# Kernel tuning notes

Hardware: AMD Instinct MI355X
Metric: run time of the kernel (lower is better)

Reference implementation:

```python
import jax, jax.numpy as jnp
import numpy as np


def _conv(x, w, pad):
    return jax.lax.conv_general_dilated(x, w, (1, 1), [(pad, pad), (pad, pad)],
                                        dimension_numbers=('NCHW', 'OIHW', 'NCHW'))


def _cbs(x, w, s, b, pad):
    # Conv + (folded inference BatchNorm as per-channel affine) + SiLU
    y = _conv(x, w, pad) * s[None, :, None, None] + b[None, :, None, None]
    return y * jax.nn.sigmoid(y)


def _pixel_shuffle(x, r):
    N, C, H, W = x.shape
    c = C // (r * r)
    return x.reshape(N, c, r, r, H, W).transpose(0, 1, 4, 2, 5, 3).reshape(N, c, H * r, W * r)


def _pixel_unshuffle(x, r):
    N, C, H, W = x.shape
    h, w = H // r, W // r
    return x.reshape(N, C, h, r, w, r).transpose(0, 1, 3, 5, 2, 4).reshape(N, C * r * r, h, w)


def _carafe(x, dw, db, ew, eb, k, up):
    # Content-aware reassembly: predict per-pixel k*k kernels for up*up sub-positions,
    # softmax-normalize, then gather-multiply-accumulate over k*k neighborhoods.
    N, C, H, W = x.shape
    kt = _conv(x, dw, 0) + db[None, :, None, None]
    if k % 2 == 0:
        kt = jnp.pad(kt, ((0, 0), (0, 0), (k // 2, k // 2 - 1), (k // 2, k // 2 - 1)))
        kt = _conv(kt, ew, 0) + eb[None, :, None, None]
    else:
        kt = _conv(kt, ew, k // 2) + eb[None, :, None, None]
    kt = _pixel_shuffle(kt, up)                     # [N, k*k, H*up, W*up]
    kt = jax.nn.softmax(kt, axis=1)
    # non-overlapping unfold(step=up) -> [N, H, W, k*k, up*up]
    kt = kt.reshape(N, k * k, H, up, W, up).transpose(0, 2, 4, 1, 3, 5).reshape(N, H, W, k * k, up * up)
    if k % 2 == 0:
        xp = jnp.pad(x, ((0, 0), (0, 0), (k // 2, k // 2 - 1), (k // 2, k // 2 - 1)))
    else:
        xp = jnp.pad(x, ((0, 0), (0, 0), (k // 2, k // 2), (k // 2, k // 2)))
    # k*k sliding patches (k is a small static constant)
    patches = jnp.stack([xp[:, :, i:i + H, j:j + W] for i in range(k) for j in range(k)], axis=-1)
    patches = patches.transpose(0, 2, 3, 1, 4)      # [N, H, W, C, k*k]
    out = jnp.einsum('nhwck,nhwkr->nhwcr', patches, kt)  # [N, H, W, C, up*up]
    out = out.reshape(N, H, W, C * up * up).transpose(0, 3, 1, 2)
    return _pixel_shuffle(out, up)


def _forward(x, cv1_w, cv1_s, cv1_b, m1a_w, m1a_s, m1a_b, m1b_w, m1b_s, m1b_b,
             cvm2_w, cvm2_s, cvm2_b, u2_down_w, u2_down_b, u2_enc_w, u2_enc_b,
             m2a_w, m2a_s, m2a_b, m2b_w, m2b_s, m2b_b,
             cvm3_w, cvm3_s, cvm3_b, u3_down_w, u3_down_b, u3_enc_w, u3_enc_b,
             m3a_w, m3a_s, m3a_b, m3b_w, m3b_s, m3b_b, cv2_w, cv2_s, cv2_b):
    C = cv1_w.shape[0] // 2
    t = _cbs(x, cv1_w, cv1_s, cv1_b, 0)
    y, y0 = t[:, :C], t[:, C:]

    def bneck(z, wa, sa, ba, wb, sb, bb):  # shortcut=False, e=1.0
        return _cbs(_cbs(z, wa, sa, ba, 1), wb, sb, bb, 1)

    y1 = bneck(y0, m1a_w, m1a_s, m1a_b, m1b_w, m1b_s, m1b_b)
    y2 = _cbs(_pixel_unshuffle(y1, 2), cvm2_w, cvm2_s, cvm2_b, 0)
    y2 = _carafe(y2, u2_down_w, u2_down_b, u2_enc_w, u2_enc_b, 1, 2) + y1
    y2 = bneck(y2, m2a_w, m2a_s, m2a_b, m2b_w, m2b_s, m2b_b)
    y3 = _cbs(_pixel_unshuffle(y2, 4), cvm3_w, cvm3_s, cvm3_b, 0)
    y3 = _carafe(y3, u3_down_w, u3_down_b, u3_enc_w, u3_enc_b, 2, 4) + y2
    y3 = bneck(y3, m3a_w, m3a_s, m3a_b, m3b_w, m3b_s, m3b_b)
    return _cbs(jnp.concatenate([y, y0, y1, y2, y3], axis=1), cv2_w, cv2_s, cv2_b, 0)


def setup_inputs() -> dict:
    key = jax.random.key(0)
    ks = jax.random.split(key, 16)
    C = 128

    def cbs_p(k, co, ci, ksz):
        k1, k2, k3 = jax.random.split(k, 3)
        w = jax.random.normal(k1, (co, ci, ksz, ksz), jnp.float32) / np.sqrt(ci * ksz * ksz).astype(np.float32)
        s = 1.0 + 0.1 * jax.random.normal(k2, (co,), jnp.float32)
        b = 0.1 * jax.random.normal(k3, (co,), jnp.float32)
        return w, s, b

    d = {}
    d['x'] = jax.random.normal(ks[0], (8, 256, 128, 128), jnp.float32)
    d['cv1_w'], d['cv1_s'], d['cv1_b'] = cbs_p(ks[1], 2 * C, 256, 1)
    for name, kk in (('m1', ks[2]), ('m2', ks[3]), ('m3', ks[4])):
        ka, kb = jax.random.split(kk)
        d[name + 'a_w'], d[name + 'a_s'], d[name + 'a_b'] = cbs_p(ka, C, C, 3)
        d[name + 'b_w'], d[name + 'b_s'], d[name + 'b_b'] = cbs_p(kb, C, C, 3)
    d['cvm2_w'], d['cvm2_s'], d['cvm2_b'] = cbs_p(ks[5], C, 4 * C, 1)
    d['cvm3_w'], d['cvm3_s'], d['cvm3_b'] = cbs_p(ks[6], C, 16 * C, 1)
    d['u2_down_w'] = jax.random.normal(ks[7], (C // 4, C, 1, 1), jnp.float32) / np.sqrt(C).astype(np.float32)
    d['u2_down_b'] = 0.1 * jax.random.normal(ks[8], (C // 4,), jnp.float32)
    d['u2_enc_w'] = jax.random.normal(ks[9], (4, C // 4, 1, 1), jnp.float32) / np.sqrt(C // 4).astype(np.float32)
    d['u2_enc_b'] = 0.1 * jax.random.normal(ks[10], (4,), jnp.float32)
    d['u3_down_w'] = jax.random.normal(ks[11], (C // 4, C, 1, 1), jnp.float32) / np.sqrt(C).astype(np.float32)
    d['u3_down_b'] = 0.1 * jax.random.normal(ks[12], (C // 4,), jnp.float32)
    d['u3_enc_w'] = jax.random.normal(ks[13], (64, C // 4, 2, 2), jnp.float32) / np.sqrt((C // 4) * 4).astype(np.float32)
    d['u3_enc_b'] = 0.1 * jax.random.normal(ks[14], (64,), jnp.float32)
    d['cv2_w'], d['cv2_s'], d['cv2_b'] = cbs_p(ks[15], 256, 5 * C, 1)
    return d


def reference(x, cv1_w, cv1_s, cv1_b, m1a_w, m1a_s, m1a_b, m1b_w, m1b_s, m1b_b,
              cvm2_w, cvm2_s, cvm2_b, u2_down_w, u2_down_b, u2_enc_w, u2_enc_b,
              m2a_w, m2a_s, m2a_b, m2b_w, m2b_s, m2b_b,
              cvm3_w, cvm3_s, cvm3_b, u3_down_w, u3_down_b, u3_enc_w, u3_enc_b,
              m3a_w, m3a_s, m3a_b, m3b_w, m3b_s, m3b_b, cv2_w, cv2_s, cv2_b):
    return _forward(x, cv1_w, cv1_s, cv1_b, m1a_w, m1a_s, m1a_b, m1b_w, m1b_s, m1b_b,
                    cvm2_w, cvm2_s, cvm2_b, u2_down_w, u2_down_b, u2_enc_w, u2_enc_b,
                    m2a_w, m2a_s, m2a_b, m2b_w, m2b_s, m2b_b,
                    cvm3_w, cvm3_s, cvm3_b, u3_down_w, u3_down_b, u3_enc_w, u3_enc_b,
                    m3a_w, m3a_s, m3a_b, m3b_w, m3b_s, m3b_b, cv2_w, cv2_s, cv2_b)
```

## Files before the change

kernel.cpp:

```cpp
#include <hip/hip_runtime.h>

typedef unsigned short u16;
typedef short v8s __attribute__((ext_vector_type(8)));
typedef u16 v8u __attribute__((ext_vector_type(8)));
typedef float v4f __attribute__((ext_vector_type(4)));
typedef __bf16 v8bf __attribute__((ext_vector_type(8)));

__device__ __forceinline__ float bf2f(u16 u) {
    unsigned x = ((unsigned)u) << 16; float f; __builtin_memcpy(&f, &x, 4); return f;
}
__device__ __forceinline__ u16 f2bf(float f) {
    unsigned x; __builtin_memcpy(&x, &f, 4);
    x = x + 0x7FFFu + ((x >> 16) & 1u);
    return (u16)(x >> 16);
}
__device__ __forceinline__ float silu(float v) { return v / (1.f + __expf(-v)); }

__device__ __forceinline__ void gld16(const void* g, void* l) {
    __builtin_amdgcn_global_load_lds(
        (const __attribute__((address_space(1))) unsigned int*)(uintptr_t)g,
        (__attribute__((address_space(3))) unsigned int*)(unsigned int)(uintptr_t)l,
        16, 0, 0);
}

__global__ void cvtw(const float* __restrict__ in, u16* __restrict__ out, int n) {
    int i = blockIdx.x * 256 + threadIdx.x;
    if (i < n) out[i] = f2bf(in[i]);
}
__global__ void wtrans3(const float* __restrict__ in, u16* __restrict__ out) {
    int i = blockIdx.x * 256 + threadIdx.x;
    if (i >= 147456) return;
    int tap = i % 9; int rem = i / 9; int ci = rem & 127; int co = rem >> 7;
    out[((tap * 128 + co) << 7) + ci] = f2bf(in[i]);
}
__global__ void wtrans_ps(const float* __restrict__ in, u16* __restrict__ out, int R2) {
    int i = blockIdx.x * 256 + threadIdx.x;
    int tap = i % R2; int rem = i / R2; int c = rem & 127; int co = rem >> 7;
    out[((tap * 128 + co) << 7) + c] = f2bf(in[i]);
}

__global__ __launch_bounds__(256) void nchw2nhwc(const float* __restrict__ in, u16* __restrict__ out) {
    __shared__ u16 tile[64][72];
    const int n = blockIdx.z, c0 = blockIdx.y * 64, p0 = blockIdx.x * 64;
#pragma unroll
    for (int rep = 0; rep < 16; ++rep) {
        int idx = rep * 256 + threadIdx.x;
        int c = idx >> 6, p = idx & 63;
        tile[c][p] = f2bf(in[((size_t)(n * 256 + c0 + c)) * 16384 + p0 + p]);
    }
    __syncthreads();
#pragma unroll
    for (int rep = 0; rep < 16; ++rep) {
        int idx = rep * 256 + threadIdx.x;
        int p = idx >> 6, c = idx & 63;
        out[((size_t)n * 16384 + p0 + p) * 256 + c0 + c] = tile[c][p];
    }
}

__global__ __launch_bounds__(256, 3) void conv3_mfma(
    const u16* __restrict__ src, int c0, int srcC,
    const u16* __restrict__ wt,
    const float* __restrict__ scale, const float* __restrict__ bias,
    u16* __restrict__ out) {
    __shared__ u16 lds[2][3][128][32];
    const int n = blockIdx.y, h = blockIdx.x;
    const int tid = threadIdx.x;
    const int lane = tid & 63;
    const int wv = tid >> 6;
    const int r = lane & 15, q = lane >> 4;
    const int wr = wv >> 1, wc = wv & 1;

    v4f acc[4][4];
#pragma unroll
    for (int a = 0; a < 4; ++a)
#pragma unroll
        for (int b = 0; b < 4; ++b) acc[a][b] = (v4f){0.f, 0.f, 0.f, 0.f};

    const size_t rowstride = (size_t)128 * srcC;
    const u16* nbase = src + (size_t)n * 128 * rowstride + c0;

    auto stage = [&](int buf, int k0) {
#pragma unroll
        for (int kh = 0; kh < 3; ++kh) {
            int hh = h + kh - 1;
            char* dst0 = (char*)&lds[buf][kh][0][0];
            if ((unsigned)hh < 128u) {
                const u16* g = nbase + (size_t)hh * rowstride + k0;
#pragma unroll
                for (int j = 0; j < 2; ++j) {
                    int o = j * 4096 + tid * 16;
                    int s2 = o ^ ((o >> 3) & 0x70);
                    int px = s2 >> 6, cb = s2 & 63;
                    gld16((const char*)(g + (size_t)px * srcC) + cb,
                          dst0 + j * 4096 + wv * 1024);
                }
            } else {
#pragma unroll
                for (int j = 0; j < 2; ++j)
                    *(v8s*)(dst0 + j * 4096 + tid * 16) = (v8s){0, 0, 0, 0, 0, 0, 0, 0};
            }
        }
    };

    stage(0, 0);
    int buf = 0;
    for (int k0 = 0; k0 < 128; k0 += 32, buf ^= 1) {
        __syncthreads();
        if (k0 + 32 < 128) stage(buf ^ 1, k0 + 32);

        const u16* wk = wt + (size_t)(wc * 64 + r) * 128 + k0 + q * 8;
        v8bf bcur[4];
#pragma unroll
        for (int nt = 0; nt < 4; ++nt)
            bcur[nt] = __builtin_bit_cast(v8bf, *(const v8s*)(wk + nt * 2048));

#pragma unroll
        for (int tap = 0; tap < 9; ++tap) {
            const int kh = tap / 3, kw = tap % 3;
            v8bf afr[4];
#pragma unroll
            for (int mt = 0; mt < 4; ++mt) {
                int p = wr * 64 + mt * 16 + r + kw - 1;
                bool vp = (unsigned)p < 128u;
                int pc = vp ? p : 0;
                int ba = pc * 64 + q * 16;
                ba ^= (ba >> 3) & 0x70;
                v8s av = *(const v8s*)((const char*)&lds[buf][kh][0][0] + ba);
                if (!vp) av = (v8s){0, 0, 0, 0, 0, 0, 0, 0};
                afr[mt] = __builtin_bit_cast(v8bf, av);
            }
            v8bf bnxt[4];
            if (tap < 8) {
#pragma unroll
                for (int nt = 0; nt < 4; ++nt)
                    bnxt[nt] = __builtin_bit_cast(v8bf,
                        *(const v8s*)(wk + (size_t)(tap + 1) * 16384 + nt * 2048));
            }
#pragma unroll
            for (int mt = 0; mt < 4; ++mt)
#pragma unroll
                for (int nt = 0; nt < 4; ++nt)
                    acc[mt][nt] = __builtin_amdgcn_mfma_f32_16x16x32_bf16(
                        afr[mt], bcur[nt], acc[mt][nt], 0, 0, 0);
            if (tap < 8) {
#pragma unroll
                for (int nt = 0; nt < 4; ++nt) bcur[nt] = bnxt[nt];
            }
        }
    }

    const size_t obase = ((size_t)n * 128 + h) * 128;
#pragma unroll
    for (int nt = 0; nt < 4; ++nt) {
        int co = wc * 64 + nt * 16 + r;
        float s = scale[co], bi = bias[co];
#pragma unroll
        for (int mt = 0; mt < 4; ++mt) {
            int p = wr * 64 + mt * 16 + q * 4;
#pragma unroll
            for (int i = 0; i < 4; ++i) {
                float v = acc[mt][nt][i] * s + bi;
                out[(obase + p + i) * 128 + co] = f2bf(silu(v));
            }
        }
    }
}

__global__ __launch_bounds__(256) void conv1_mfma(
    const u16* __restrict__ src, int srcC,
    const u16* __restrict__ wt,
    const float* __restrict__ scale, const float* __restrict__ bias,
    u16* __restrict__ out, int Cout) {
    __shared__ u16 lds[2][128][64];
    const int n = blockIdx.z, co0 = blockIdx.y * 128, px0 = blockIdx.x * 128;
    const int tid = threadIdx.x;
    const int lane = tid & 63, wv = tid >> 6;
    const int r = lane & 15, q = lane >> 4;
    const int wr = wv >> 1, wc = wv & 1;

    v4f acc[4][4];
#pragma unroll
    for (int a = 0; a < 4; ++a)
#pragma unroll
        for (int b = 0; b < 4; ++b) acc[a][b] = (v4f){0.f, 0.f, 0.f, 0.f};

    const u16* abase = src + ((size_t)n * 16384 + px0) * srcC;

    auto stage = [&](int buf, int k0) {
#pragma unroll
        for (int j = 0; j < 4; ++j) {
            int o = j * 4096 + tid * 16;
            int s2 = o ^ ((o >> 3) & 0x70);
            int px = s2 >> 7, cb = s2 & 127;
            gld16((const char*)(abase + (size_t)px * srcC + k0) + cb,
                  (char*)&lds[buf][0][0] + j * 4096 + wv * 1024);
        }
    };

    stage(0, 0);
    int buf = 0;
    for (int k0 = 0; k0 < srcC; k0 += 64, buf ^= 1) {
        __syncthreads();
        if (k0 + 64 < srcC) stage(buf ^ 1, k0 + 64);

        const u16* wrow = wt + (size_t)(co0 + wc * 64 + r) * srcC + k0 + q * 8;
        v8bf bfr[2][4];
#pragma unroll
        for (int s = 0; s < 2; ++s)
#pragma unroll
            for (int nt = 0; nt < 4; ++nt)
                bfr[s][nt] = __builtin_bit_cast(v8bf,
                    *(const v8s*)(wrow + s * 32 + (size_t)nt * 16 * srcC));
#pragma unroll
        for (int s = 0; s < 2; ++s) {
            v8bf afr[4];
#pragma unroll
            for (int mt = 0; mt < 4; ++mt) {
                int ba = (wr * 64 + mt * 16 + r) * 128 + s * 64 + q * 16;
                ba ^= (ba >> 3) & 0x70;
                afr[mt] = __builtin_bit_cast(v8bf,
                    *(const v8s*)((const char*)&lds[buf][0][0] + ba));
            }
#pragma unroll
            for (int mt = 0; mt < 4; ++mt)
#pragma unroll
                for (int nt = 0; nt < 4; ++nt)
                    acc[mt][nt] = __builtin_amdgcn_mfma_f32_16x16x32_bf16(
                        afr[mt], bfr[s][nt], acc[mt][nt], 0, 0, 0);
        }
    }

#pragma unroll
    for (int nt = 0; nt < 4; ++nt) {
        int co = co0 + wc * 64 + nt * 16 + r;
        float s = scale[co], bi = bias[co];
#pragma unroll
        for (int mt = 0; mt < 4; ++mt) {
            int p = px0 + wr * 64 + mt * 16 + q * 4;
#pragma unroll
            for (int i = 0; i < 4; ++i) {
                float v = acc[mt][nt][i] * s + bi;
                out[((size_t)n * 16384 + p + i) * Cout + co] = f2bf(silu(v));
            }
        }
    }
}

__global__ __launch_bounds__(256) void cat_mfma(
    const u16* __restrict__ s0, const u16* __restrict__ s1,
    const u16* __restrict__ s2, const u16* __restrict__ s3,
    const u16* __restrict__ wt,
    const float* __restrict__ scale, const float* __restrict__ bias,
    float* __restrict__ out) {
    __shared__ u16 lds[2][128][64];
    const int n = blockIdx.z, co0 = blockIdx.y * 128, px0 = blockIdx.x * 128;
    const int tid = threadIdx.x;
    const int lane = tid & 63, wv = tid >> 6;
    const int r = lane & 15, q = lane >> 4;
    const int wr = wv >> 1, wc = wv & 1;

    v4f acc[4][4];
#pragma unroll
    for (int a = 0; a < 4; ++a)
#pragma unroll
        for (int b = 0; b < 4; ++b) acc[a][b] = (v4f){0.f, 0.f, 0.f, 0.f};

    const u16* srcs[4] = {s0, s1, s2, s3};
    const int sCq[4] = {256, 128, 128, 128};
    const int kbq[4] = {0, 256, 384, 512};
    const int segs[10] = {0, 0, 0, 0, 1, 1, 2, 2, 3, 3};
    const int k0s[10] = {0, 64, 128, 192, 0, 64, 0, 64, 0, 64};

    auto stage = [&](int buf, int c) {
        int seg = segs[c]; int sc = sCq[seg]; int k0 = k0s[c];
        const u16* ab = srcs[seg] + ((size_t)n * 16384 + px0) * sc;
#pragma unroll
        for (int j = 0; j < 4; ++j) {
            int o = j * 4096 + tid * 16;
            int s2 = o ^ ((o >> 3) & 0x70);
            int px = s2 >> 7, cb = s2 & 127;
            gld16((const char*)(ab + (size_t)px * sc + k0) + cb,
                  (char*)&lds[buf][0][0] + j * 4096 + wv * 1024);
        }
    };

    stage(0, 0);
    int buf = 0;
#pragma unroll
    for (int c = 0; c < 10; ++c, buf ^= 1) {
        __syncthreads();
        if (c < 9) stage(buf ^ 1, c + 1);

        const int seg = segs[c], k0 = k0s[c];
        const u16* wrow = wt + (size_t)(co0 + wc * 64 + r) * 640 + kbq[seg] + k0 + q * 8;
        v8bf bfr[2][4];
#pragma unroll
        for (int s = 0; s < 2; ++s)
#pragma unroll
            for (int nt = 0; nt < 4; ++nt)
                bfr[s][nt] = __builtin_bit_cast(v8bf,
                    *(const v8s*)(wrow + s * 32 + (size_t)nt * 16 * 640));
#pragma unroll
        for (int s = 0; s < 2; ++s) {
            v8bf afr[4];
#pragma unroll
            for (int mt = 0; mt < 4; ++mt) {
                int ba = (wr * 64 + mt * 16 + r) * 128 + s * 64 + q * 16;
                ba ^= (ba >> 3) & 0x70;
                afr[mt] = __builtin_bit_cast(v8bf,
                    *(const v8s*)((const char*)&lds[buf][0][0] + ba));
            }
#pragma unroll
            for (int mt = 0; mt < 4; ++mt)
#pragma unroll
                for (int nt = 0; nt < 4; ++nt)
                    acc[mt][nt] = __builtin_amdgcn_mfma_f32_16x16x32_bf16(
                        afr[mt], bfr[s][nt], acc[mt][nt], 0, 0, 0);
        }
    }

#pragma unroll
    for (int nt = 0; nt < 4; ++nt) {
        int co = co0 + wc * 64 + nt * 16 + r;
        float s = scale[co], bi = bias[co];
#pragma unroll
        for (int mt = 0; mt < 4; ++mt) {
            int p = px0 + wr * 64 + mt * 16 + q * 4;
            v4f o;
#pragma unroll
            for (int i = 0; i < 4; ++i) o[i] = silu(acc[mt][nt][i] * s + bi);
            *(v4f*)(out + (size_t)(n * 256 + co) * 16384 + p) = o;
        }
    }
}

template <int KH, int KW, int S, int PAD, int CIN>
__global__ __launch_bounds__(256) void conv_mfma(
    const u16* __restrict__ src, int c0, int srcC,
    const u16* __restrict__ wt,
    const float* __restrict__ scale, const float* __restrict__ bias,
    u16* __restrict__ out, int Hin, int Win, int Wout, int Cout) {
    const int n = blockIdx.z;
    const int co0 = blockIdx.y * 64;
    const int hw0 = blockIdx.x * 64;
    const int tid = threadIdx.x;
    const int lane = tid & 63, wv = tid >> 6;
    const int r = lane & 15, q = lane >> 4;
    const int wr = wv >> 1, wc = wv & 1;

    const int m0 = hw0 + wr * 32 + r;
    const int m1 = m0 + 16;
    const int h0 = m0 / Wout, w0 = m0 - h0 * Wout;
    const int h1 = m1 / Wout, w1 = m1 - h1 * Wout;

    v4f acc00 = {0.f, 0.f, 0.f, 0.f}, acc01 = {0.f, 0.f, 0.f, 0.f};
    v4f acc10 = {0.f, 0.f, 0.f, 0.f}, acc11 = {0.f, 0.f, 0.f, 0.f};

    const u16* b0base = wt + (size_t)(co0 + wc * 32 + r) * CIN + q * 8;
    const size_t wtap = (size_t)Cout * CIN;

    int tap = 0;
#pragma unroll
    for (int kh = 0; kh < KH; ++kh)
#pragma unroll
        for (int kw = 0; kw < KW; ++kw, ++tap) {
            int ih0 = h0 * S + kh - PAD, iw0 = w0 * S + kw - PAD;
            int ih1 = h1 * S + kh - PAD, iw1 = w1 * S + kw - PAD;
            bool v0 = ((unsigned)ih0 < (unsigned)Hin) & ((unsigned)iw0 < (unsigned)Win);
            bool v1 = ((unsigned)ih1 < (unsigned)Hin) & ((unsigned)iw1 < (unsigned)Win);
            int p0i = v0 ? (n * Hin + ih0) * Win + iw0 : 0;
            int p1i = v1 ? (n * Hin + ih1) * Win + iw1 : 0;
            const u16* a0 = src + (size_t)p0i * srcC + c0 + q * 8;
            const u16* a1 = src + (size_t)p1i * srcC + c0 + q * 8;
            const u16* b0 = b0base + (size_t)tap * wtap;
            const u16* b1 = b0 + (size_t)16 * CIN;
#pragma unroll
            for (int k = 0; k < CIN; k += 32) {
                v8s za = {0, 0, 0, 0, 0, 0, 0, 0};
                v8s a0s = za, a1s = za;
                if (v0) a0s = *(const v8s*)(a0 + k);
                if (v1) a1s = *(const v8s*)(a1 + k);
                v8s b0s = *(const v8s*)(b0 + k);
                v8s b1s = *(const v8s*)(b1 + k);
                v8bf af0 = __builtin_bit_cast(v8bf, a0s);
                v8bf af1 = __builtin_bit_cast(v8bf, a1s);
                v8bf bw0 = __builtin_bit_cast(v8bf, b0s);
                v8bf bw1 = __builtin_bit_cast(v8bf, b1s);
                acc00 = __builtin_amdgcn_mfma_f32_16x16x32_bf16(af0, bw0, acc00, 0, 0, 0);
                acc01 = __builtin_amdgcn_mfma_f32_16x16x32_bf16(af0, bw1, acc01, 0, 0, 0);
                acc10 = __builtin_amdgcn_mfma_f32_16x16x32_bf16(af1, bw0, acc10, 0, 0, 0);
                acc11 = __builtin_amdgcn_mfma_f32_16x16x32_bf16(af1, bw1, acc11, 0, 0, 0);
            }
        }

    const int HWo = gridDim.x * 64;
#pragma unroll
    for (int ct = 0; ct < 2; ++ct) {
        v4f av0 = ct ? acc01 : acc00;
        v4f av1 = ct ? acc11 : acc10;
        int co = co0 + wc * 32 + ct * 16 + r;
        float s = scale[co], bb = bias[co];
        int mb = hw0 + wr * 32 + q * 4;
#pragma unroll
        for (int i = 0; i < 4; ++i) {
            float x0 = av0[i] * s + bb;
            float x1 = av1[i] * s + bb;
            out[((size_t)n * HWo + mb + i) * Cout + co] = f2bf(silu(x0));
            out[((size_t)n * HWo + mb + 16 + i) * Cout + co] = f2bf(silu(x1));
        }
    }
}

__global__ __launch_bounds__(256) void k_upadd(const u16* __restrict__ y2a,
                                               const u16* __restrict__ y1,
                                               u16* __restrict__ out) {
    int t = blockIdx.x * 256 + threadIdx.x;
    int cg = t & 15; int pix = t >> 4;
    int n = pix >> 14; int p = pix & 16383; int ho = p >> 7; int wo = p & 127;
    const u16* a = y2a + ((size_t)((n * 64 + (ho >> 1)) * 64 + (wo >> 1))) * 128 + cg * 8;
    const u16* b = y1 + (size_t)pix * 128 + cg * 8;
    v8s av = *(const v8s*)a;
    v8s bv = *(const v8s*)b;
    v8u o;
#pragma unroll
    for (int e = 0; e < 8; ++e) o[e] = f2bf(bf2f((u16)av[e]) + bf2f((u16)bv[e]));
    *(v8u*)(out + (size_t)pix * 128 + cg * 8) = o;
}

__global__ __launch_bounds__(256) void k_u3down(const u16* __restrict__ y3a,
                                                const float* __restrict__ w,
                                                const float* __restrict__ b,
                                                float* __restrict__ ktA) {
    int t = blockIdx.x * 256 + threadIdx.x;
    int co = t & 31; int pix = t >> 5;
    const u16* xr = y3a + (size_t)pix * 128;
    const float* wr = w + (size_t)co * 128;
    float acc = b[co];
#pragma unroll 16
    for (int k = 0; k < 128; ++k) acc += bf2f(xr[k]) * wr[k];
    ktA[t] = acc;
}

__global__ __launch_bounds__(256) void k_u3enc(const float* __restrict__ ktA,
                                               const float* __restrict__ ew,
                                               const float* __restrict__ eb,
                                               float* __restrict__ wtsm) {
    int t = blockIdx.x * 256 + threadIdx.x;
    int r = t & 15; int pix = t >> 4;
    int n = pix >> 10; int hw = pix & 1023; int h = hw >> 5; int w = hw & 31;
    float v[4];
#pragma unroll
    for (int kk = 0; kk < 4; ++kk) {
        int co = kk * 16 + r;
        float acc = eb[co];
#pragma unroll
        for (int dh = 0; dh < 2; ++dh)
#pragma unroll
            for (int dw = 0; dw < 2; ++dw) {
                int hh = h - 1 + dh, ww = w - 1 + dw;
                if (hh < 0 || ww < 0) continue;
                const float* kp = ktA + ((size_t)((n * 32 + hh) * 32 + ww)) * 32;
                const float* wp = ew + (size_t)co * 128 + dh * 2 + dw;
                for (int ci = 0; ci < 32; ++ci) acc += kp[ci] * wp[ci * 4];
            }
        v[kk] = acc;
    }
    float mx = fmaxf(fmaxf(v[0], v[1]), fmaxf(v[2], v[3]));
    float e0 = __expf(v[0] - mx), e1 = __expf(v[1] - mx), e2 = __expf(v[2] - mx), e3 = __expf(v[3] - mx);
    float inv = 1.f / (e0 + e1 + e2 + e3);
    float* o = wtsm + (size_t)t * 4;
    o[0] = e0 * inv; o[1] = e1 * inv; o[2] = e2 * inv; o[3] = e3 * inv;
}

__global__ __launch_bounds__(256) void k_carafe(const u16* __restrict__ y3a,
                                                const float* __restrict__ wtsm,
                                                const u16* __restrict__ y2,
                                                u16* __restrict__ out) {
    int t = blockIdx.x * 256 + threadIdx.x;
    int cg = t & 15; int pix = t >> 4;
    int n = pix >> 14; int p = pix & 16383; int ho = p >> 7; int wo = p & 127;
    int h = ho >> 2, i = ho & 3, w = wo >> 2, j = wo & 3, r = i * 4 + j;
    const float* wv = wtsm + ((size_t)((n * 1024 + h * 32 + w) * 16 + r)) * 4;
    v8s yv = *(const v8s*)(y2 + (size_t)pix * 128 + cg * 8);
    float acc[8];
#pragma unroll
    for (int e = 0; e < 8; ++e) acc[e] = bf2f((u16)yv[e]);
#pragma unroll
    for (int kk = 0; kk < 4; ++kk) {
        int ki = kk >> 1, kj = kk & 1;
        int hh = h + ki - 1, ww = w + kj - 1;
        if (hh < 0 || ww < 0) continue;
        float wk = wv[kk];
        v8s sv = *(const v8s*)(y3a + ((size_t)((n * 32 + hh) * 32 + ww)) * 128 + cg * 8);
#pragma unroll
        for (int e = 0; e < 8; ++e) acc[e] += wk * bf2f((u16)sv[e]);
    }
    v8u o;
#pragma unroll
    for (int e = 0; e < 8; ++e) o[e] = f2bf(acc[e]);
    *(v8u*)(out + (size_t)pix * 128 + cg * 8) = o;
}

extern "C" void kernel_launch(void* const* d_in, const int* in_sizes, int n_in,
                              void* d_out, int out_size, void* d_ws, size_t ws_size,
                              hipStream_t stream) {
    const float* x     = (const float*)d_in[0];
    const float* cv1_w = (const float*)d_in[1];
    const float* cv1_s = (const float*)d_in[2];
    const float* cv1_b = (const float*)d_in[3];
    const float* m1a_w = (const float*)d_in[4];
    const float* m1a_s = (const float*)d_in[5];
    const float* m1a_b = (const float*)d_in[6];
    const float* m1b_w = (const float*)d_in[7];
    const float* m1b_s = (const float*)d_in[8];
    const float* m1b_b = (const float*)d_in[9];
    const float* m2a_w = (const float*)d_in[10];
    const float* m2a_s = (const float*)d_in[11];
    const float* m2a_b = (const float*)d_in[12];
    const float* m2b_w = (const float*)d_in[13];
    const float* m2b_s = (const float*)d_in[14];
    const float* m2b_b = (const float*)d_in[15];
    const float* m3a_w = (const float*)d_in[16];
    const float* m3a_s = (const float*)d_in[17];
    const float* m3a_b = (const float*)d_in[18];
    const float* m3b_w = (const float*)d_in[19];
    const float* m3b_s = (const float*)d_in[20];
    const float* m3b_b = (const float*)d_in[21];
    const float* cvm2_w = (const float*)d_in[22];
    const float* cvm2_s = (const float*)d_in[23];
    const float* cvm2_b = (const float*)d_in[24];
    const float* cvm3_w = (const float*)d_in[25];
    const float* cvm3_s = (const float*)d_in[26];
    const float* cvm3_b = (const float*)d_in[27];
    const float* u3_down_w = (const float*)d_in[32];
    const float* u3_down_b = (const float*)d_in[33];
    const float* u3_enc_w  = (const float*)d_in[34];
    const float* u3_enc_b  = (const float*)d_in[35];
    const float* cv2_w = (const float*)d_in[36];
    const float* cv2_s = (const float*)d_in[37];
    const float* cv2_b = (const float*)d_in[38];

    char* ws = (char*)d_ws;
    u16* A    = (u16*)(ws + 0);
    u16* t    = (u16*)(ws + 67108864);
    u16* y1   = (u16*)(ws + 134217728);
    u16* bt   = (u16*)(ws + 167772160);
    u16* te   = (u16*)(ws + 201326592);
    u16* y2a  = (u16*)(ws + 234881024);
    u16* y3a  = (u16*)(ws + 243269632);
    float* ktA = (float*)(ws + 245366784);
    float* wts = (float*)(ws + 246415360);
    u16* w3t  = (u16*)(ws + 248512512);
    u16* wu2  = (u16*)(ws + 250281984);
    u16* wu4  = (u16*)(ws + 250413056);
    u16* wc1  = (u16*)(ws + 250937344);
    u16* wc2  = (u16*)(ws + 251068416);
    u16* y2 = A;
    u16* y3 = A + 16777216;

    dim3 B(256);
    wtrans3<<<576, B, 0, stream>>>(m1a_w, w3t + 0 * 147456);
    wtrans3<<<576, B, 0, stream>>>(m1b_w, w3t + 1 * 147456);
    wtrans3<<<576, B, 0, stream>>>(m2a_w, w3t + 2 * 147456);
    wtrans3<<<576, B, 0, stream>>>(m2b_w, w3t + 3 * 147456);
    wtrans3<<<576, B, 0, stream>>>(m3a_w, w3t + 4 * 147456);
    wtrans3<<<576, B, 0, stream>>>(m3b_w, w3t + 5 * 147456);
    wtrans_ps<<<256, B, 0, stream>>>(cvm2_w, wu2, 4);
    wtrans_ps<<<1024, B, 0, stream>>>(cvm3_w, wu4, 16);
    cvtw<<<256, B, 0, stream>>>(cv1_w, wc1, 65536);
    cvtw<<<640, B, 0, stream>>>(cv2_w, wc2, 163840);

    nchw2nhwc<<<dim3(256, 4, 8), B, 0, stream>>>(x, A);

    conv1_mfma<<<dim3(128, 2, 8), B, 0, stream>>>(A, 256, wc1, cv1_s, cv1_b, t, 256);

    conv3_mfma<<<dim3(128, 8), B, 0, stream>>>(t, 128, 256, w3t + 0 * 147456, m1a_s, m1a_b, bt);
    conv3_mfma<<<dim3(128, 8), B, 0, stream>>>(bt, 0, 128, w3t + 1 * 147456, m1b_s, m1b_b, y1);

    conv_mfma<2, 2, 2, 0, 128><<<dim3(64, 2, 8), B, 0, stream>>>(
        y1, 0, 128, wu2, cvm2_s, cvm2_b, y2a, 128, 128, 64, 128);

    k_upadd<<<8192, B, 0, stream>>>(y2a, y1, te);

    conv3_mfma<<<dim3(128, 8), B, 0, stream>>>(te, 0, 128, w3t + 2 * 147456, m2a_s, m2a_b, bt);
    conv3_mfma<<<dim3(128, 8), B, 0, stream>>>(bt, 0, 128, w3t + 3 * 147456, m2b_s, m2b_b, y2);

    conv_mfma<4, 4, 4, 0, 128><<<dim3(16, 2, 8), B, 0, stream>>>(
        y2, 0, 128, wu4, cvm3_s, cvm3_b, y3a, 128, 128, 32, 128);

    k_u3down<<<1024, B, 0, stream>>>(y3a, u3_down_w, u3_down_b, ktA);
    k_u3enc<<<512, B, 0, stream>>>(ktA, u3_enc_w, u3_enc_b, wts);
    k_carafe<<<8192, B, 0, stream>>>(y3a, wts, y2, te);

    conv3_mfma<<<dim3(128, 8), B, 0, stream>>>(te, 0, 128, w3t + 4 * 147456, m3a_s, m3a_b, bt);
    conv3_mfma<<<dim3(128, 8), B, 0, stream>>>(bt, 0, 128, w3t + 5 * 147456, m3b_s, m3b_b, y3);

    cat_mfma<<<dim3(128, 2, 8), B, 0, stream>>>(t, y1, y2, y3, wc2, cv2_s, cv2_b, (float*)d_out);
}
```

Before: 1.378 ms.

## Restage conv3 K in halves, prefetch weights, coalesce outputs through LDS

```diff
diff --git a/kernel.cpp b/kernel.cpp
--- a/kernel.cpp
+++ b/kernel.cpp
@@ -57,13 +57,15 @@
     }
 }
 
-__global__ __launch_bounds__(256, 3) void conv3_mfma(
+__global__ __launch_bounds__(256, 2) void conv3_mfma(
     const u16* __restrict__ src, int c0, int srcC,
     const u16* __restrict__ wt,
     const float* __restrict__ scale, const float* __restrict__ bias,
     u16* __restrict__ out) {
-    __shared__ u16 lds[2][3][128][32];
-    const int n = blockIdx.y, h = blockIdx.x;
+    __shared__ __align__(16) char smem[49152];
+    const int n = blockIdx.y;
+    const int hraw = blockIdx.x;
+    const int h = ((hraw & 7) << 4) | (hraw >> 3);
     const int tid = threadIdx.x;
     const int lane = tid & 63;
     const int wv = tid >> 6;
@@ -79,90 +81,100 @@
     const size_t rowstride = (size_t)128 * srcC;
     const u16* nbase = src + (size_t)n * 128 * rowstride + c0;
 
-    auto stage = [&](int buf, int k0) {
-#pragma unroll
-        for (int kh = 0; kh < 3; ++kh) {
+    auto stage = [&](int koff) {
+#pragma unroll
+        for (int j = 0; j < 12; ++j) {
+            int t = wv * 12 + j;
+            int kh = t >> 4;
             int hh = h + kh - 1;
-            char* dst0 = (char*)&lds[buf][kh][0][0];
+            char* dst = smem + t * 1024;
             if ((unsigned)hh < 128u) {
-                const u16* g = nbase + (size_t)hh * rowstride + k0;
-#pragma unroll
-                for (int j = 0; j < 2; ++j) {
-                    int o = j * 4096 + tid * 16;
-                    int s2 = o ^ ((o >> 3) & 0x70);
-                    int px = s2 >> 6, cb = s2 & 63;
-                    gld16((const char*)(g + (size_t)px * srcC) + cb,
-                          dst0 + j * 4096 + wv * 1024);
-                }
+                int px = ((t & 15) << 3) + (lane >> 3);
+                int cb = (lane & 7) * 16;
+                cb ^= (px & 7) << 4;
+                const char* g = (const char*)(nbase + (size_t)hh * rowstride + koff)
+                                + (size_t)px * srcC * 2 + cb;
+                gld16(g, dst);
             } else {
-#pragma unroll
-                for (int j = 0; j < 2; ++j)
-                    *(v8s*)(dst0 + j * 4096 + tid * 16) = (v8s){0, 0, 0, 0, 0, 0, 0, 0};
+                *(v8s*)(dst + lane * 16) = (v8s){0, 0, 0, 0, 0, 0, 0, 0};
             }
         }
     };
 
-    stage(0, 0);
-    int buf = 0;
-    for (int k0 = 0; k0 < 128; k0 += 32, buf ^= 1) {
-        __syncthreads();
-        if (k0 + 32 < 128) stage(buf ^ 1, k0 + 32);
-
-        const u16* wk = wt + (size_t)(wc * 64 + r) * 128 + k0 + q * 8;
-        v8bf bcur[4];
-#pragma unroll
-        for (int nt = 0; nt < 4; ++nt)
-            bcur[nt] = __builtin_bit_cast(v8bf, *(const v8s*)(wk + nt * 2048));
-
-#pragma unroll
-        for (int tap = 0; tap < 9; ++tap) {
-            const int kh = tap / 3, kw = tap % 3;
+    auto loadB = [&](v8bf (&B)[12], int kh, int koff, int k0l) {
+#pragma unroll
+        for (int kw = 0; kw < 3; ++kw)
+#pragma unroll
+            for (int nt = 0; nt < 4; ++nt)
+                B[kw * 4 + nt] = __builtin_bit_cast(v8bf, *(const v8s*)(
+                    wt + (size_t)((kh * 3 + kw) * 128 + wc * 64 + nt * 16 + r) * 128
+                       + koff + k0l + q * 8));
+    };
+
+    auto comp = [&](v8bf (&B)[12], int kh, int k0l) {
+#pragma unroll
+        for (int kw = 0; kw < 3; ++kw) {
             v8bf afr[4];
 #pragma unroll
             for (int mt = 0; mt < 4; ++mt) {
                 int p = wr * 64 + mt * 16 + r + kw - 1;
                 bool vp = (unsigned)p < 128u;
                 int pc = vp ? p : 0;
-                int ba = pc * 64 + q * 16;
-                ba ^= (ba >> 3) & 0x70;
-                v8s av = *(const v8s*)((const char*)&lds[buf][kh][0][0] + ba);
+                int o = kh * 16384 + pc * 128 + k0l * 2 + q * 16;
+                o ^= (pc & 7) << 4;
+                v8s av = *(const v8s*)(smem + o);
                 if (!vp) av = (v8s){0, 0, 0, 0, 0, 0, 0, 0};
                 afr[mt] = __builtin_bit_cast(v8bf, av);
             }
-            v8bf bnxt[4];
-            if (tap < 8) {
-#pragma unroll
-                for (int nt = 0; nt < 4; ++nt)
-                    bnxt[nt] = __builtin_bit_cast(v8bf,
-                        *(const v8s*)(wk + (size_t)(tap + 1) * 16384 + nt * 2048));
-            }
 #pragma unroll
             for (int mt = 0; mt < 4; ++mt)
 #pragma unroll
                 for (int nt = 0; nt < 4; ++nt)
                     acc[mt][nt] = __builtin_amdgcn_mfma_f32_16x16x32_bf16(
-                        afr[mt], bcur[nt], acc[mt][nt], 0, 0, 0);
-            if (tap < 8) {
-#pragma unroll
-                for (int nt = 0; nt < 4; ++nt) bcur[nt] = bnxt[nt];
-            }
-        }
-    }
-
-    const size_t obase = ((size_t)n * 128 + h) * 128;
+                        afr[mt], B[kw * 4 + nt], acc[mt][nt], 0, 0, 0);
+        }
+    };
+
+#pragma unroll
+    for (int hf = 0; hf < 2; ++hf) {
+        const int koff = hf * 64;
+        __syncthreads();
+        stage(koff);
+        __syncthreads();
+#pragma unroll
+        for (int k0l = 0; k0l < 64; k0l += 32) {
+            v8bf bA[12], bB[12];
+            loadB(bA, 0, koff, k0l);
+            loadB(bB, 1, koff, k0l);
+            comp(bA, 0, k0l);
+            loadB(bA, 2, koff, k0l);
+            comp(bB, 1, k0l);
+            comp(bA, 2, k0l);
+        }
+    }
+
+    __syncthreads();
+    u16* ldsO = (u16*)smem;
 #pragma unroll
     for (int nt = 0; nt < 4; ++nt) {
         int co = wc * 64 + nt * 16 + r;
         float s = scale[co], bi = bias[co];
 #pragma unroll
         for (int mt = 0; mt < 4; ++mt) {
-            int p = wr * 64 + mt * 16 + q * 4;
 #pragma unroll
             for (int i = 0; i < 4; ++i) {
-                float v = acc[mt][nt][i] * s + bi;
-                out[(obase + p + i) * 128 + co] = f2bf(silu(v));
-            }
-        }
+                int p = wr * 64 + mt * 16 + q * 4 + i;
+                ldsO[p * 136 + co] = f2bf(silu(acc[mt][nt][i] * s + bi));
+            }
+        }
+    }
+    __syncthreads();
+    const size_t obase = ((size_t)n * 128 + h) * 128;
+#pragma unroll
+    for (int rep = 0; rep < 8; ++rep) {
+        int px = rep * 16 + (tid >> 4);
+        int c8 = (tid & 15) * 8;
+        *(v8u*)(out + (obase + px) * 128 + c8) = *(const v8u*)&ldsO[px * 136 + c8];
     }
 }
 
@@ -171,7 +183,7 @@
     const u16* __restrict__ wt,
     const float* __restrict__ scale, const float* __restrict__ bias,
     u16* __restrict__ out, int Cout) {
-    __shared__ u16 lds[2][128][64];
+    __shared__ __align__(16) char smem[34816];
     const int n = blockIdx.z, co0 = blockIdx.y * 128, px0 = blockIdx.x * 128;
     const int tid = threadIdx.x;
     const int lane = tid & 63, wv = tid >> 6;
@@ -193,56 +205,76 @@
             int s2 = o ^ ((o >> 3) & 0x70);
             int px = s2 >> 7, cb = s2 & 127;
             gld16((const char*)(abase + (size_t)px * srcC + k0) + cb,
-                  (char*)&lds[buf][0][0] + j * 4096 + wv * 1024);
+                  smem + buf * 16384 + j * 4096 + wv * 1024);
         }
     };
-
+    auto loadB = [&](v8bf (&B)[2][4], int k0) {
+        const u16* wrow = wt + (size_t)(co0 + wc * 64 + r) * srcC + k0 + q * 8;
+#pragma unroll
+        for (int s = 0; s < 2; ++s)
+#pragma unroll
+            for (int nt = 0; nt < 4; ++nt)
+                B[s][nt] = __builtin_bit_cast(v8bf,
+                    *(const v8s*)(wrow + s * 32 + (size_t)nt * 16 * srcC));
+    };
+
+    v8bf bcur[2][4], bnxt[2][4];
+    loadB(bcur, 0);
     stage(0, 0);
     int buf = 0;
     for (int k0 = 0; k0 < srcC; k0 += 64, buf ^= 1) {
         __syncthreads();
-        if (k0 + 64 < srcC) stage(buf ^ 1, k0 + 64);
-
-        const u16* wrow = wt + (size_t)(co0 + wc * 64 + r) * srcC + k0 + q * 8;
-        v8bf bfr[2][4];
-#pragma unroll
-        for (int s = 0; s < 2; ++s)
-#pragma unroll
-            for (int nt = 0; nt < 4; ++nt)
-                bfr[s][nt] = __builtin_bit_cast(v8bf,
-                    *(const v8s*)(wrow + s * 32 + (size_t)nt * 16 * srcC));
+        bool more = (k0 + 64 < srcC);
+        if (more) {
+            loadB(bnxt, k0 + 64);
+            stage(buf ^ 1, k0 + 64);
+        }
 #pragma unroll
         for (int s = 0; s < 2; ++s) {
             v8bf afr[4];
 #pragma unroll
             for (int mt = 0; mt < 4; ++mt) {
-                int ba = (wr * 64 + mt * 16 + r) * 128 + s * 64 + q * 16;
+                int ba = buf * 16384 + (wr * 64 + mt * 16 + r) * 128 + s * 64 + q * 16;
                 ba ^= (ba >> 3) & 0x70;
-                afr[mt] = __builtin_bit_cast(v8bf,
-                    *(const v8s*)((const char*)&lds[buf][0][0] + ba));
+                afr[mt] = __builtin_bit_cast(v8bf, *(const v8s*)(smem + ba));
             }
 #pragma unroll
             for (int mt = 0; mt < 4; ++mt)
 #pragma unroll
                 for (int nt = 0; nt < 4; ++nt)
                     acc[mt][nt] = __builtin_amdgcn_mfma_f32_16x16x32_bf16(
-                        afr[mt], bfr[s][nt], acc[mt][nt], 0, 0, 0);
-        }
-    }
-
+                        afr[mt], bcur[s][nt], acc[mt][nt], 0, 0, 0);
+        }
+        if (more) {
+#pragma unroll
+            for (int s = 0; s < 2; ++s)
+#pragma unroll
+                for (int nt = 0; nt < 4; ++nt) bcur[s][nt] = bnxt[s][nt];
+        }
+    }
+
+    __syncthreads();
+    u16* ldsO = (u16*)smem;
 #pragma unroll
     for (int nt = 0; nt < 4; ++nt) {
         int co = co0 + wc * 64 + nt * 16 + r;
         float s = scale[co], bi = bias[co];
 #pragma unroll
         for (int mt = 0; mt < 4; ++mt) {
-            int p = px0 + wr * 64 + mt * 16 + q * 4;
 #pragma unroll
             for (int i = 0; i < 4; ++i) {
-                float v = acc[mt][nt][i] * s + bi;
-                out[((size_t)n * 16384 + p + i) * Cout + co] = f2bf(silu(v));
-            }
-        }
+                int p = wr * 64 + mt * 16 + q * 4 + i;
+                ldsO[p * 136 + (wc * 64 + nt * 16 + r)] = f2bf(silu(acc[mt][nt][i] * s + bi));
+            }
+        }
+    }
+    __syncthreads();
+#pragma unroll
+    for (int rep = 0; rep < 8; ++rep) {
+        int px = rep * 16 + (tid >> 4);
+        int c8 = (tid & 15) * 8;
+        *(v8u*)(out + ((size_t)n * 16384 + px0 + px) * Cout + co0 + c8) =
+            *(const v8u*)&ldsO[px * 136 + c8];
     }
 }
 
@@ -252,7 +284,7 @@
     const u16* __restrict__ wt,
     const float* __restrict__ scale, const float* __restrict__ bias,
     float* __restrict__ out) {
-    __shared__ u16 lds[2][128][64];
+    __shared__ __align__(16) u16 lds[2][128][64];
     const int n = blockIdx.z, co0 = blockIdx.y * 128, px0 = blockIdx.x * 128;
     const int tid = threadIdx.x;
     const int lane = tid & 63, wv = tid >> 6;
@@ -283,23 +315,27 @@
                   (char*)&lds[buf][0][0] + j * 4096 + wv * 1024);
         }
     };
-
+    auto loadB = [&](v8bf (&B)[2][4], int c) {
+        const u16* wrow = wt + (size_t)(co0 + wc * 64 + r) * 640 + kbq[segs[c]] + k0s[c] + q * 8;
+#pragma unroll
+        for (int s = 0; s < 2; ++s)
+#pragma unroll
+            for (int nt = 0; nt < 4; ++nt)
+                B[s][nt] = __builtin_bit_cast(v8bf,
+                    *(const v8s*)(wrow + s * 32 + (size_t)nt * 16 * 640));
+    };
+
+    v8bf bcur[2][4], bnxt[2][4];
+    loadB(bcur, 0);
     stage(0, 0);
     int buf = 0;
 #pragma unroll
     for (int c = 0; c < 10; ++c, buf ^= 1) {
         __syncthreads();
-        if (c < 9) stage(buf ^ 1, c + 1);
-
-        const int seg = segs[c], k0 = k0s[c];
-        const u16* wrow = wt + (size_t)(co0 + wc * 64 + r) * 640 + kbq[seg] + k0 + q * 8;
-        v8bf bfr[2][4];
-#pragma unroll
-        for (int s = 0; s < 2; ++s)
-#pragma unroll
-            for (int nt = 0; nt < 4; ++nt)
-                bfr[s][nt] = __builtin_bit_cast(v8bf,
-                    *(const v8s*)(wrow + s * 32 + (size_t)nt * 16 * 640));
+        if (c < 9) {
+            loadB(bnxt, c + 1);
+            stage(buf ^ 1, c + 1);
+        }
 #pragma unroll
         for (int s = 0; s < 2; ++s) {
             v8bf afr[4];
@@ -315,7 +351,13 @@
 #pragma unroll
                 for (int nt = 0; nt < 4; ++nt)
                     acc[mt][nt] = __builtin_amdgcn_mfma_f32_16x16x32_bf16(
-                        afr[mt], bfr[s][nt], acc[mt][nt], 0, 0, 0);
+                        afr[mt], bcur[s][nt], acc[mt][nt], 0, 0, 0);
+        }
+        if (c < 9) {
+#pragma unroll
+            for (int s = 0; s < 2; ++s)
+#pragma unroll
+                for (int nt = 0; nt < 4; ++nt) bcur[s][nt] = bnxt[s][nt];
         }
     }
 
```

Measured after the change: 1.388 ms. Within noise of the previous version (+0.7%).
